# Kernel tuning notes

Hardware: AMD Instinct MI355X
Metric: run time of the kernel (lower is better)

## Reference

```python
import jax, jax.numpy as jnp
import numpy as np

N_NODES = 50000
N_EDGES = 800000
D = 128  # in_dim == hidden_dim


def setup_inputs() -> dict:
    key = jax.random.key(0)
    k1, k2, k3, k4 = jax.random.split(key, 4)
    x = jax.random.normal(k1, (N_NODES, D), dtype=jnp.float32)
    edge_index = jax.random.randint(k2, (2, N_EDGES), 0, N_NODES, dtype=jnp.int64)
    # Glorot-ish scale for square weights
    scale = 1.0 / np.sqrt(D)
    W1 = jax.random.normal(k3, (D, D), dtype=jnp.float32) * scale
    W2 = jax.random.normal(k4, (D, D), dtype=jnp.float32) * scale
    b1 = jnp.zeros((D,), dtype=jnp.float32)
    b2 = jnp.zeros((D,), dtype=jnp.float32)
    return {"x": x, "edge_index": edge_index, "W1": W1, "b1": b1, "W2": W2, "b2": b2}


def _gcn_layer(x, W, b, src, dst, norm, n):
    # PyG GCNConv: h = x @ W, then symmetric-normalized scatter-add, then + bias
    h = x @ W                                   # [N, D] dense GEMM
    msg = h[src] * norm[:, None]                # [E', D] gather + scale
    out = jax.ops.segment_sum(msg, dst, num_segments=n)  # scatter-add
    return out + b


def reference(x, edge_index, W1, b1, W2, b2):
    n = x.shape[0]
    # add self-loops (GCNConv default add_self_loops=True)
    loops = jnp.arange(n, dtype=edge_index.dtype)
    src = jnp.concatenate([edge_index[0], loops])
    dst = jnp.concatenate([edge_index[1], loops])
    # symmetric normalization: deg^{-1/2}[src] * deg^{-1/2}[dst]
    deg = jax.ops.segment_sum(jnp.ones_like(src, dtype=x.dtype), dst, num_segments=n)
    dinv = jax.lax.rsqrt(jnp.maximum(deg, 1.0))  # deg >= 1 due to self-loops
    norm = dinv[src] * dinv[dst]
    # layer 1: conv -> relu (dropout is identity in eval mode)
    h = jax.nn.relu(_gcn_layer(x, W1, b1, src, dst, norm, n))
    # layer 2 (cut='c2'): conv -> relu
    h = jax.nn.relu(_gcn_layer(h, W2, b2, src, dst, norm, n))
    return h
```

## Files before the change

kernel.cpp:

```cpp
#include <hip/hip_runtime.h>

#define NN 50000
#define NE 800000
#define DD 128
#define NSTRIP 3125
#define NB 196
#define CHUNK 4096
#define MAXB 6144

#define OF_LCNT  0
#define OF_LOFS  50176
#define OF_DINV  100352
#define OF_OFFS2 150352
#define OF_TMP2  250352
#define OF_CSRU  1053168
#define OF_H1    1655280
#define OF_H2    4855280
#define OF_W1H   8055280
#define OF_W1L   8063472
#define OF_W2H   8071664
#define OF_W2L   8079856

typedef __attribute__((ext_vector_type(8))) short bf8_t;
typedef __attribute__((ext_vector_type(8))) unsigned short us8;
typedef __attribute__((ext_vector_type(4))) float f32x4;

static __device__ __forceinline__ unsigned short f2bf(float f) {
    unsigned int u = __float_as_uint(f);
    unsigned int r = (u + 0x7fffu + ((u >> 16) & 1u)) >> 16;
    return (unsigned short)r;
}
static __device__ __forceinline__ float bf2f(unsigned short h) {
    return __uint_as_float(((unsigned int)h) << 16);
}

__global__ __launch_bounds__(256) void k_ws(
        const float* __restrict__ W1, const float* __restrict__ W2,
        ushort* __restrict__ w1h, ushort* __restrict__ w1l,
        ushort* __restrict__ w2h, ushort* __restrict__ w2l,
        const int* __restrict__ src, const int* __restrict__ dst,
        int* __restrict__ lcnt_g, int* __restrict__ lofs_g,
        unsigned int* __restrict__ tmp2) {
    __shared__ int lcnt[256];
    __shared__ int lsc[256];
    __shared__ int lcur[256];
    int tid = threadIdx.x;
    if (blockIdx.x < 16) {
        int gg = blockIdx.x * 256 + tid;
        const float* W = (gg < 2048) ? W1 : W2;
        ushort* wh = (gg < 2048) ? w1h : w2h;
        ushort* wl = (gg < 2048) ? w1l : w2l;
        int g = gg & 2047;
        int ntile = g >> 8;
        int kk = (g >> 6) & 3;
        int lane = g & 63;
        int k0 = kk * 32 + ((lane >> 4) * 8);
        int col = ntile * 16 + (lane & 15);
#pragma unroll
        for (int j = 0; j < 8; ++j) {
            float w = W[(k0 + j) * DD + col];
            unsigned short h = f2bf(w);
            wh[(size_t)g * 8 + j] = h;
            wl[(size_t)g * 8 + j] = f2bf(w - bf2f(h));
        }
        return;
    }
    int blk = blockIdx.x - 16;
    lcnt[tid] = 0;
    __syncthreads();
    int e0 = blk * CHUNK;
    int e1 = e0 + CHUNK; if (e1 > NE) e1 = NE;
    for (int e = e0 + tid; e < e1; e += 256)
        atomicAdd(&lcnt[dst[e] >> 8], 1);
    __syncthreads();
    int v = lcnt[tid];
    lsc[tid] = v;
    __syncthreads();
    for (int o = 1; o < 256; o <<= 1) {
        int t = (tid >= o) ? lsc[tid - o] : 0;
        __syncthreads();
        lsc[tid] += t;
        __syncthreads();
    }
    int excl = lsc[tid] - v;
    lcnt_g[tid * 196 + blk] = v;
    lofs_g[tid * 196 + blk] = excl;
    lcur[tid] = excl;
    __syncthreads();
    for (int e = e0 + tid; e < e1; e += 256) {
        int d = dst[e], s = src[e];
        int b = d >> 8;
        int r = atomicAdd(&lcur[b], 1);
        tmp2[blk * CHUNK + r] = ((unsigned int)s << 8) | (unsigned int)(d & 255);
    }
}

__global__ __launch_bounds__(256) void k_sg(
        const int* __restrict__ lcnt_g, const int* __restrict__ lofs_g,
        const unsigned int* __restrict__ tmp2,
        ushort* __restrict__ csru, int2* __restrict__ offs2,
        float* __restrict__ dinv,
        const float* __restrict__ X,
        const ushort* __restrict__ wh, const ushort* __restrict__ wl,
        ushort* __restrict__ H1) {
    __shared__ unsigned int ent[MAXB];
    __shared__ int c[256];
    __shared__ int p[256];
    __shared__ int o[256];
    __shared__ int cnt[256];
    __shared__ int boff[256];
    __shared__ int cur[256];
    int tid = threadIdx.x;
    if (blockIdx.x < 196) {
        int b = blockIdx.x;
        int cv = (tid < 196) ? lcnt_g[b * 196 + tid] : 0;
        o[tid] = (tid < 196) ? lofs_g[b * 196 + tid] : 0;
        c[tid] = cv;
        p[tid] = cv;
        cnt[tid] = 0;
        __syncthreads();
        for (int s = 1; s < 256; s <<= 1) {
            int t = (tid >= s) ? p[tid - s] : 0;
            __syncthreads();
            p[tid] += t;
            __syncthreads();
        }
        int nb = p[255];
        for (int i = tid; i < nb; i += 256) {
            int lo = 0, hi = 255;
#pragma unroll
            for (int it = 0; it < 8; ++it) {
                int mid = (lo + hi) >> 1;
                if (p[mid] > i) hi = mid; else lo = mid + 1;
            }
            int blk = lo;
            int j = i - (p[blk] - c[blk]);
            unsigned int e = tmp2[blk * CHUNK + o[blk] + j];
            ent[i] = e;
            atomicAdd(&cnt[e & 255], 1);
        }
        __syncthreads();
        int v = cnt[tid];
        boff[tid] = v;
        __syncthreads();
        for (int s = 1; s < 256; s <<= 1) {
            int t = (tid >= s) ? boff[tid - s] : 0;
            __syncthreads();
            boff[tid] += t;
            __syncthreads();
        }
        int excl = boff[tid] - v;
        int base = b * MAXB;
        int node = b * 256 + tid;
        if (node < NN) {
            offs2[node] = make_int2(base + excl, base + excl + v);
            dinv[node] = rsqrtf((float)(v + 1));
        }
        cur[tid] = excl;
        __syncthreads();
        for (int i = tid; i < nb; i += 256) {
            unsigned int e = ent[i];
            int bin = e & 255;
            int r = atomicAdd(&cur[bin], 1);
            csru[base + r] = (ushort)(e >> 8);
        }
        return;
    }
    int wave = tid >> 6;
    int lane = tid & 63;
    int strip = (blockIdx.x - 196) * 4 + wave;
    if (strip >= NSTRIP) return;
    int rb = strip << 4;
    int m = lane & 15;
    int quad = lane >> 4;
    const float* ar = X + (size_t)(rb + m) * DD;
    f32x4 acc[8];
#pragma unroll
    for (int t = 0; t < 8; ++t) acc[t] = (f32x4){0.f, 0.f, 0.f, 0.f};
#pragma unroll
    for (int kk = 0; kk < 4; ++kk) {
        float4 xa = *(const float4*)(ar + kk * 32 + quad * 8);
        float4 xb = *(const float4*)(ar + kk * 32 + quad * 8 + 4);
        float xs[8] = {xa.x, xa.y, xa.z, xa.w, xb.x, xb.y, xb.z, xb.w};
        bf8_t ah, al;
#pragma unroll
        for (int j = 0; j < 8; ++j) {
            unsigned short hh = f2bf(xs[j]);
            ah[j] = (short)hh;
            al[j] = (short)f2bf(xs[j] - bf2f(hh));
        }
#pragma unroll
        for (int t = 0; t < 8; ++t) {
            size_t bo = ((size_t)(t * 4 + kk) * 64 + lane) * 8;
            bf8_t bh = *(const bf8_t*)(wh + bo);
            bf8_t bl = *(const bf8_t*)(wl + bo);
            acc[t] = __builtin_amdgcn_mfma_f32_16x16x32_bf16(ah, bh, acc[t], 0, 0, 0);
            acc[t] = __builtin_amdgcn_mfma_f32_16x16x32_bf16(ah, bl, acc[t], 0, 0, 0);
            acc[t] = __builtin_amdgcn_mfma_f32_16x16x32_bf16(al, bh, acc[t], 0, 0, 0);
        }
    }
#pragma unroll
    for (int t = 0; t < 8; ++t) {
#pragma unroll
        for (int r = 0; r < 4; ++r)
            H1[(size_t)(rb + quad * 4 + r) * DD + t * 16 + m] = f2bf(acc[t][r]);
    }
}

__global__ __launch_bounds__(512) void k_aggmm(const ushort* __restrict__ h1,
                                               const float* __restrict__ dinv,
                                               const int2* __restrict__ offs2,
                                               const ushort* __restrict__ csru,
                                               const float* __restrict__ b1,
                                               const ushort* __restrict__ w2h,
                                               const ushort* __restrict__ w2l,
                                               ushort* __restrict__ h2) {
    __shared__ float xs[16][136];
    int wave = threadIdx.x >> 6;
    int lane = threadIdx.x & 63;
    int rb = blockIdx.x * 16;
    int q = lane >> 4;
    int l = lane & 15;
    const float* bp = b1 + 8 * l;
    for (int nn = 0; nn < 2; ++nn) {
        int node = rb + wave * 2 + nn;
        int2 oe = offs2[node];
        int e1 = oe.y;
        float a[8] = {0.f, 0.f, 0.f, 0.f, 0.f, 0.f, 0.f, 0.f};
        for (int eb = oe.x; eb < e1; eb += 32) {
            int s[8]; float w[8];
#pragma unroll
            for (int j = 0; j < 8; ++j) {
                int e = eb + q + 4 * j;
                int er = (e < e1) ? e : (e1 - 1);
                er = (er < 0) ? 0 : er;
                s[j] = (int)csru[er];
                w[j] = (e < e1) ? dinv[s[j]] : 0.f;
            }
            us8 v[8];
#pragma unroll
            for (int j = 0; j < 8; ++j)
                v[j] = *(const us8*)(h1 + ((size_t)s[j] << 7) + 8 * l);
#pragma unroll
            for (int j = 0; j < 8; ++j) {
#pragma unroll
                for (int d = 0; d < 8; ++d) a[d] += w[j] * bf2f(v[j][d]);
            }
        }
        float dnode = dinv[node];
        if (q == 0) {
            us8 v = *(const us8*)(h1 + ((size_t)node << 7) + 8 * l);
#pragma unroll
            for (int j = 0; j < 8; ++j) a[j] += dnode * bf2f(v[j]);
        }
#pragma unroll
        for (int j = 0; j < 8; ++j) {
            a[j] += __shfl_xor(a[j], 16, 64);
            a[j] += __shfl_xor(a[j], 32, 64);
        }
        if (q == 0) {
            float* xr = &xs[wave * 2 + nn][8 * l];
#pragma unroll
            for (int j = 0; j < 8; ++j)
                xr[j] = fmaxf(dnode * a[j] + bp[j], 0.f);
        }
    }
    __syncthreads();
    int m = lane & 15;
    int quad = lane >> 4;
    int t = wave;
    f32x4 acc = (f32x4){0.f, 0.f, 0.f, 0.f};
#pragma unroll
    for (int kk = 0; kk < 4; ++kk) {
        const float* xr = &xs[m][kk * 32 + quad * 8];
        float4 xa = *(const float4*)xr;
        float4 xb = *(const float4*)(xr + 4);
        float xv[8] = {xa.x, xa.y, xa.z, xa.w, xb.x, xb.y, xb.z, xb.w};
        bf8_t ah, al;
#pragma unroll
        for (int j = 0; j < 8; ++j) {
            unsigned short hh = f2bf(xv[j]);
            ah[j] = (short)hh;
            al[j] = (short)f2bf(xv[j] - bf2f(hh));
        }
        size_t bo = ((size_t)(t * 4 + kk) * 64 + lane) * 8;
        bf8_t bh = *(const bf8_t*)(w2h + bo);
        bf8_t bl = *(const bf8_t*)(w2l + bo);
        acc = __builtin_amdgcn_mfma_f32_16x16x32_bf16(ah, bh, acc, 0, 0, 0);
        acc = __builtin_amdgcn_mfma_f32_16x16x32_bf16(ah, bl, acc, 0, 0, 0);
        acc = __builtin_amdgcn_mfma_f32_16x16x32_bf16(al, bh, acc, 0, 0, 0);
    }
#pragma unroll
    for (int r = 0; r < 4; ++r)
        h2[(size_t)(rb + quad * 4 + r) * DD + t * 16 + m] = f2bf(acc[r]);
}

__global__ __launch_bounds__(256) void k_agg(const ushort* __restrict__ h,
                                             const float* __restrict__ dinv,
                                             const int2* __restrict__ offs2,
                                             const ushort* __restrict__ csru,
                                             const float* __restrict__ bias,
                                             float* __restrict__ outf) {
    int wave = threadIdx.x >> 6;
    int lane = threadIdx.x & 63;
    int node = blockIdx.x * 4 + wave;
    int q = lane >> 4;
    int l = lane & 15;
    int2 oe = offs2[node];
    int e1 = oe.y;
    float a[8] = {0.f, 0.f, 0.f, 0.f, 0.f, 0.f, 0.f, 0.f};
    for (int eb = oe.x; eb < e1; eb += 32) {
        int s[8]; float w[8];
#pragma unroll
        for (int j = 0; j < 8; ++j) {
            int e = eb + q + 4 * j;
            int er = (e < e1) ? e : (e1 - 1);
            er = (er < 0) ? 0 : er;
            s[j] = (int)csru[er];
            w[j] = (e < e1) ? dinv[s[j]] : 0.f;
        }
        us8 v[8];
#pragma unroll
        for (int j = 0; j < 8; ++j)
            v[j] = *(const us8*)(h + ((size_t)s[j] << 7) + 8 * l);
#pragma unroll
        for (int j = 0; j < 8; ++j) {
#pragma unroll
            for (int d = 0; d < 8; ++d) a[d] += w[j] * bf2f(v[j][d]);
        }
    }
    float dnode = dinv[node];
    if (q == 0) {
        us8 v = *(const us8*)(h + ((size_t)node << 7) + 8 * l);
#pragma unroll
        for (int j = 0; j < 8; ++j) a[j] += dnode * bf2f(v[j]);
    }
#pragma unroll
    for (int j = 0; j < 8; ++j) {
        a[j] += __shfl_xor(a[j], 16, 64);
        a[j] += __shfl_xor(a[j], 32, 64);
    }
    if (q == 0) {
        float* op = outf + (size_t)node * DD + 8 * l;
        const float* bp = bias + 8 * l;
        float4 o0, o1;
        o0.x = fmaxf(dnode * a[0] + bp[0], 0.f);
        o0.y = fmaxf(dnode * a[1] + bp[1], 0.f);
        o0.z = fmaxf(dnode * a[2] + bp[2], 0.f);
        o0.w = fmaxf(dnode * a[3] + bp[3], 0.f);
        o1.x = fmaxf(dnode * a[4] + bp[4], 0.f);
        o1.y = fmaxf(dnode * a[5] + bp[5], 0.f);
        o1.z = fmaxf(dnode * a[6] + bp[6], 0.f);
        o1.w = fmaxf(dnode * a[7] + bp[7], 0.f);
        *(float4*)op = o0;
        *(float4*)(op + 4) = o1;
    }
}

extern "C" void kernel_launch(void* const* d_in, const int* in_sizes, int n_in,
                              void* d_out, int out_size, void* d_ws, size_t ws_size,
                              hipStream_t stream) {
    const float* x  = (const float*)d_in[0];
    const int*   ei = (const int*)d_in[1];
    const float* W1 = (const float*)d_in[2];
    const float* b1 = (const float*)d_in[3];
    const float* W2 = (const float*)d_in[4];
    const float* b2 = (const float*)d_in[5];
    float* out = (float*)d_out;

    const int* src = ei;
    const int* dst = ei + NE;

    int*          wsi  = (int*)d_ws;
    float*        wsf  = (float*)d_ws;
    ushort*       wsu  = (ushort*)d_ws;
    unsigned int* wsuw = (unsigned int*)d_ws;
    int*    lcnt_g = wsi + OF_LCNT;
    int*    lofs_g = wsi + OF_LOFS;
    float*  dinv   = wsf + OF_DINV;
    int2*   offs2  = (int2*)(wsi + OF_OFFS2);
    unsigned int* tmp2 = wsuw + OF_TMP2;
    ushort* csru   = wsu + (size_t)OF_CSRU * 2;
    ushort* h1     = wsu + (size_t)OF_H1 * 2;
    ushort* h2     = wsu + (size_t)OF_H2 * 2;
    ushort* w1h    = wsu + (size_t)OF_W1H * 2;
    ushort* w1l    = wsu + (size_t)OF_W1L * 2;
    ushort* w2h    = wsu + (size_t)OF_W2H * 2;
    ushort* w2l    = wsu + (size_t)OF_W2L * 2;

    hipLaunchKernelGGL(k_ws, dim3(16 + 196), dim3(256), 0, stream,
                       W1, W2, w1h, w1l, w2h, w2l,
                       src, dst, lcnt_g, lofs_g, tmp2);
    hipLaunchKernelGGL(k_sg, dim3(196 + (NSTRIP + 3) / 4), dim3(256), 0, stream,
                       lcnt_g, lofs_g, tmp2, csru, offs2, dinv,
                       x, w1h, w1l, h1);
    hipLaunchKernelGGL(k_aggmm, dim3(NSTRIP), dim3(512), 0, stream,
                       h1, dinv, offs2, csru, b1, w2h, w2l, h2);
    hipLaunchKernelGGL(k_agg, dim3(NN / 4), dim3(256), 0, stream,
                       h2, dinv, offs2, csru, b2, out);
}
```

Before: 220.3 us.

## Pre-scale GEMM outputs by source dinv and store as fp16

The source-side normalization dinv[src] is folded into the GEMM epilogues, so h1 and h2 rows are stored already scaled, using fp16 instead of bf16. Degrees are computed with global atomics in the bucketing kernel so the first GEMM can apply rsqrt directly. The aggregation loops no longer gather dinv per edge, and out-of-range lanes point at a zeroed padding row instead of being masked by weight. In exchange this adds a zeroing kernel, global atomics on deg, and fp16 range and precision risk on the stored features.

Measured after the change: 217.3 us. No clear change (-1.4%).

```diff
diff --git a/kernel.cpp b/kernel.cpp
--- a/kernel.cpp
+++ b/kernel.cpp
@@ -1,4 +1,5 @@
 #include <hip/hip_runtime.h>
+#include <hip/hip_fp16.h>
 
 #define NN 50000
 #define NE 800000
@@ -7,19 +8,21 @@
 #define NB 196
 #define CHUNK 4096
 #define MAXB 6144
+#define ZROW NN
 
 #define OF_LCNT  0
 #define OF_LOFS  50176
 #define OF_DINV  100352
-#define OF_OFFS2 150352
-#define OF_TMP2  250352
-#define OF_CSRU  1053168
-#define OF_H1    1655280
-#define OF_H2    4855280
-#define OF_W1H   8055280
-#define OF_W1L   8063472
-#define OF_W2H   8071664
-#define OF_W2L   8079856
+#define OF_DEG   150352
+#define OF_OFFS2 200352
+#define OF_TMP2  300352
+#define OF_CSRU  1103168
+#define OF_H1    1705280
+#define OF_H2    4905344
+#define OF_W1H   8105408
+#define OF_W1L   8113600
+#define OF_W2H   8121792
+#define OF_W2L   8129984
 
 typedef __attribute__((ext_vector_type(8))) short bf8_t;
 typedef __attribute__((ext_vector_type(8))) unsigned short us8;
@@ -32,6 +35,21 @@
 }
 static __device__ __forceinline__ float bf2f(unsigned short h) {
     return __uint_as_float(((unsigned int)h) << 16);
+}
+static __device__ __forceinline__ unsigned short f2h(float f) {
+    return __half_as_ushort(__float2half(f));
+}
+static __device__ __forceinline__ float h2f(unsigned short u) {
+    return __half2float(__ushort_as_half(u));
+}
+
+__global__ __launch_bounds__(256) void k_zero(int* __restrict__ deg,
+                                              ushort* __restrict__ h1,
+                                              ushort* __restrict__ h2) {
+    int g = blockIdx.x * 256 + threadIdx.x;
+    if (g < NN) deg[g] = 0;
+    if (g < 64) ((unsigned int*)(h1 + (size_t)ZROW * DD))[g] = 0u;
+    else if (g < 128) ((unsigned int*)(h2 + (size_t)ZROW * DD))[g - 64] = 0u;
 }
 
 __global__ __launch_bounds__(256) void k_ws(
@@ -40,7 +58,7 @@
         ushort* __restrict__ w2h, ushort* __restrict__ w2l,
         const int* __restrict__ src, const int* __restrict__ dst,
         int* __restrict__ lcnt_g, int* __restrict__ lofs_g,
-        unsigned int* __restrict__ tmp2) {
+        unsigned int* __restrict__ tmp2, int* __restrict__ deg) {
     __shared__ int lcnt[256];
     __shared__ int lsc[256];
     __shared__ int lcur[256];
@@ -70,8 +88,11 @@
     __syncthreads();
     int e0 = blk * CHUNK;
     int e1 = e0 + CHUNK; if (e1 > NE) e1 = NE;
-    for (int e = e0 + tid; e < e1; e += 256)
-        atomicAdd(&lcnt[dst[e] >> 8], 1);
+    for (int e = e0 + tid; e < e1; e += 256) {
+        int d = dst[e];
+        atomicAdd(&lcnt[d >> 8], 1);
+        atomicAdd(&deg[d], 1);
+    }
     __syncthreads();
     int v = lcnt[tid];
     lsc[tid] = v;
@@ -97,7 +118,7 @@
 
 __global__ __launch_bounds__(256) void k_sg(
         const int* __restrict__ lcnt_g, const int* __restrict__ lofs_g,
-        const unsigned int* __restrict__ tmp2,
+        const unsigned int* __restrict__ tmp2, const int* __restrict__ deg,
         ushort* __restrict__ csru, int2* __restrict__ offs2,
         float* __restrict__ dinv,
         const float* __restrict__ X,
@@ -199,11 +220,15 @@
             acc[t] = __builtin_amdgcn_mfma_f32_16x16x32_bf16(al, bh, acc[t], 0, 0, 0);
         }
     }
+    int4 dg = *(const int4*)(deg + rb + quad * 4);
+    float dvv[4] = {rsqrtf((float)(dg.x + 1)), rsqrtf((float)(dg.y + 1)),
+                    rsqrtf((float)(dg.z + 1)), rsqrtf((float)(dg.w + 1))};
 #pragma unroll
     for (int t = 0; t < 8; ++t) {
 #pragma unroll
         for (int r = 0; r < 4; ++r)
-            H1[(size_t)(rb + quad * 4 + r) * DD + t * 16 + m] = f2bf(acc[t][r]);
+            H1[(size_t)(rb + quad * 4 + r) * DD + t * 16 + m] =
+                f2h(dvv[r] * acc[t][r]);
     }
 }
 
@@ -228,14 +253,14 @@
         int e1 = oe.y;
         float a[8] = {0.f, 0.f, 0.f, 0.f, 0.f, 0.f, 0.f, 0.f};
         for (int eb = oe.x; eb < e1; eb += 32) {
-            int s[8]; float w[8];
+            int s[8];
 #pragma unroll
             for (int j = 0; j < 8; ++j) {
                 int e = eb + q + 4 * j;
                 int er = (e < e1) ? e : (e1 - 1);
                 er = (er < 0) ? 0 : er;
-                s[j] = (int)csru[er];
-                w[j] = (e < e1) ? dinv[s[j]] : 0.f;
+                int sv = (int)csru[er];
+                s[j] = (e < e1) ? sv : ZROW;
             }
             us8 v[8];
 #pragma unroll
@@ -244,14 +269,13 @@
 #pragma unroll
             for (int j = 0; j < 8; ++j) {
 #pragma unroll
-                for (int d = 0; d < 8; ++d) a[d] += w[j] * bf2f(v[j][d]);
+                for (int d = 0; d < 8; ++d) a[d] += h2f(v[j][d]);
             }
         }
-        float dnode = dinv[node];
         if (q == 0) {
             us8 v = *(const us8*)(h1 + ((size_t)node << 7) + 8 * l);
 #pragma unroll
-            for (int j = 0; j < 8; ++j) a[j] += dnode * bf2f(v[j]);
+            for (int j = 0; j < 8; ++j) a[j] += h2f(v[j]);
         }
 #pragma unroll
         for (int j = 0; j < 8; ++j) {
@@ -259,6 +283,7 @@
             a[j] += __shfl_xor(a[j], 32, 64);
         }
         if (q == 0) {
+            float dnode = dinv[node];
             float* xr = &xs[wave * 2 + nn][8 * l];
 #pragma unroll
             for (int j = 0; j < 8; ++j)
@@ -290,9 +315,11 @@
         acc = __builtin_amdgcn_mfma_f32_16x16x32_bf16(ah, bl, acc, 0, 0, 0);
         acc = __builtin_amdgcn_mfma_f32_16x16x32_bf16(al, bh, acc, 0, 0, 0);
     }
+    float4 dv4 = *(const float4*)(dinv + rb + quad * 4);
+    float dvv[4] = {dv4.x, dv4.y, dv4.z, dv4.w};
 #pragma unroll
     for (int r = 0; r < 4; ++r)
-        h2[(size_t)(rb + quad * 4 + r) * DD + t * 16 + m] = f2bf(acc[r]);
+        h2[(size_t)(rb + quad * 4 + r) * DD + t * 16 + m] = f2h(dvv[r] * acc[r]);
 }
 
 __global__ __launch_bounds__(256) void k_agg(const ushort* __restrict__ h,
@@ -310,14 +337,14 @@
     int e1 = oe.y;
     float a[8] = {0.f, 0.f, 0.f, 0.f, 0.f, 0.f, 0.f, 0.f};
     for (int eb = oe.x; eb < e1; eb += 32) {
-        int s[8]; float w[8];
+        int s[8];
 #pragma unroll
         for (int j = 0; j < 8; ++j) {
             int e = eb + q + 4 * j;
             int er = (e < e1) ? e : (e1 - 1);
             er = (er < 0) ? 0 : er;
-            s[j] = (int)csru[er];
-            w[j] = (e < e1) ? dinv[s[j]] : 0.f;
+            int sv = (int)csru[er];
+            s[j] = (e < e1) ? sv : ZROW;
         }
         us8 v[8];
 #pragma unroll
@@ -326,14 +353,13 @@
 #pragma unroll
         for (int j = 0; j < 8; ++j) {
 #pragma unroll
-            for (int d = 0; d < 8; ++d) a[d] += w[j] * bf2f(v[j][d]);
-        }
-    }
-    float dnode = dinv[node];
+            for (int d = 0; d < 8; ++d) a[d] += h2f(v[j][d]);
+        }
+    }
     if (q == 0) {
         us8 v = *(const us8*)(h + ((size_t)node << 7) + 8 * l);
 #pragma unroll
-        for (int j = 0; j < 8; ++j) a[j] += dnode * bf2f(v[j]);
+        for (int j = 0; j < 8; ++j) a[j] += h2f(v[j]);
     }
 #pragma unroll
     for (int j = 0; j < 8; ++j) {
@@ -341,6 +367,7 @@
         a[j] += __shfl_xor(a[j], 32, 64);
     }
     if (q == 0) {
+        float dnode = dinv[node];
         float* op = outf + (size_t)node * DD + 8 * l;
         const float* bp = bias + 8 * l;
         float4 o0, o1;
@@ -378,6 +405,7 @@
     int*    lcnt_g = wsi + OF_LCNT;
     int*    lofs_g = wsi + OF_LOFS;
     float*  dinv   = wsf + OF_DINV;
+    int*    deg    = wsi + OF_DEG;
     int2*   offs2  = (int2*)(wsi + OF_OFFS2);
     unsigned int* tmp2 = wsuw + OF_TMP2;
     ushort* csru   = wsu + (size_t)OF_CSRU * 2;
@@ -388,11 +416,12 @@
     ushort* w2h    = wsu + (size_t)OF_W2H * 2;
     ushort* w2l    = wsu + (size_t)OF_W2L * 2;
 
+    hipLaunchKernelGGL(k_zero, dim3(196), dim3(256), 0, stream, deg, h1, h2);
     hipLaunchKernelGGL(k_ws, dim3(16 + 196), dim3(256), 0, stream,
                        W1, W2, w1h, w1l, w2h, w2l,
-                       src, dst, lcnt_g, lofs_g, tmp2);
+                       src, dst, lcnt_g, lofs_g, tmp2, deg);
     hipLaunchKernelGGL(k_sg, dim3(196 + (NSTRIP + 3) / 4), dim3(256), 0, stream,
-                       lcnt_g, lofs_g, tmp2, csru, offs2, dinv,
+                       lcnt_g, lofs_g, tmp2, deg, csru, offs2, dinv,
                        x, w1h, w1l, h1);
     hipLaunchKernelGGL(k_aggmm, dim3(NSTRIP), dim3(512), 0, stream,
                        h1, dinv, offs2, csru, b1, w2h, w2l, h2);
```
